# Performance work log

Measured on AMD Instinct MI355X. Metric: run time of the kernel, lower is better.

Reference implementation:

```python
import jax, jax.numpy as jnp
import numpy as np

EMB = 1024

def setup_inputs() -> dict:
    key = jax.random.key(0)
    ks = jax.random.split(key, 6)
    B, S, E = 4, 2048, EMB
    x = jax.random.normal(ks[0], (B, S, E), dtype=jnp.float32)
    attention_mask = jax.random.randint(ks[1], (B, S, S), 0, 2, dtype=jnp.int32)
    proj_w = jax.random.normal(ks[2], (E, 3 * E), dtype=jnp.float32) * (1.0 / np.sqrt(E))
    proj_b = jax.random.normal(ks[3], (3 * E,), dtype=jnp.float32) * 0.02
    out_w = jax.random.normal(ks[4], (E, E), dtype=jnp.float32) * (1.0 / np.sqrt(E))
    out_b = jax.random.normal(ks[5], (E,), dtype=jnp.float32) * 0.02
    return {"x": x, "attention_mask": attention_mask, "proj_w": proj_w,
            "proj_b": proj_b, "out_w": out_w, "out_b": out_b}

def reference(x, attention_mask, proj_w, proj_b, out_w, out_b):
    E = x.shape[-1]
    scale = 1.0 / jnp.sqrt(jnp.asarray(E, x.dtype))
    qkv = x @ proj_w + proj_b                      # [B,S,3E]
    q, k, v = jnp.split(qkv, 3, axis=-1)           # each [B,S,E]
    scores = jnp.einsum('bqe,bke->bqk', q, k) * scale  # [B,S,S]
    scores = jnp.where(attention_mask == 0, jnp.asarray(-1e20, scores.dtype), scores)
    attn = jax.nn.softmax(scores, axis=-1)
    ctx = jnp.einsum('bqk,bke->bqe', attn, v)      # [B,S,E]
    return ctx @ out_w + out_b
```

## Files before the change

### kernel.cpp

```cpp
#include <hip/hip_runtime.h>
#include <cstdint>

typedef unsigned short u16;
typedef uint32_t u32;
typedef __bf16 bf16x8 __attribute__((ext_vector_type(8)));
typedef float f32x4 __attribute__((ext_vector_type(4)));

__device__ __forceinline__ u16 f2bf(float f) {
  unsigned u = __float_as_uint(f);
  u += 0x7fffu + ((u >> 16) & 1u);
  return (u16)(u >> 16);
}

__device__ __forceinline__ void async16(const void* g, void* l) {
  __builtin_amdgcn_global_load_lds(
      (const __attribute__((address_space(1))) uint32_t*)g,
      (__attribute__((address_space(3))) uint32_t*)l, 16, 0, 0);
}

__global__ __launch_bounds__(256) void k_prep(const float* __restrict__ x, u16* __restrict__ xb,
                                              const float* __restrict__ pw, u16* __restrict__ wt,
                                              const float* __restrict__ ow, u16* __restrict__ owt,
                                              const int* __restrict__ mask, u32* __restrict__ mbits) {
  const int bid = blockIdx.x;
  if (bid < 8192) {
    const int i = bid * 256 + threadIdx.x;
    const float4 v = ((const float4*)x)[i];
    ushort4 o;
    o.x = f2bf(v.x); o.y = f2bf(v.y); o.z = f2bf(v.z); o.w = f2bf(v.w);
    ((ushort4*)xb)[i] = o;
    return;
  }
  if (bid >= 12288) {
    const size_t w = (size_t)(bid - 12288) * 256 + threadIdx.x;
    const int* p = mask + w * 32;
    u32 bits = 0;
#pragma unroll
    for (int j = 0; j < 8; ++j) {
      const int4 v = ((const int4*)p)[j];
      bits |= (u32)(v.x & 1) << (j * 4 + 0);
      bits |= (u32)(v.y & 1) << (j * 4 + 1);
      bits |= (u32)(v.z & 1) << (j * 4 + 2);
      bits |= (u32)(v.w & 1) << (j * 4 + 3);
    }
    mbits[w] = bits;
    return;
  }
  __shared__ u16 tile[32][33];
  const int tx = threadIdx.x & 31, ty = threadIdx.x >> 5;
  const float* in;
  u16* outp;
  int lda, ldo, c0, r0;
  if (bid < 11264) {
    const int id = bid - 8192;
    c0 = (id % 96) * 32; r0 = (id / 96) * 32;
    in = pw; outp = wt; lda = 3072; ldo = 1024;
  } else {
    const int id = bid - 11264;
    c0 = (id % 32) * 32; r0 = (id / 32) * 32;
    in = ow; outp = owt; lda = 1024; ldo = 1024;
  }
#pragma unroll
  for (int i = 0; i < 4; ++i)
    tile[ty + i * 8][tx] = f2bf(in[(size_t)(r0 + ty + i * 8) * lda + c0 + tx]);
  __syncthreads();
#pragma unroll
  for (int i = 0; i < 4; ++i)
    outp[(size_t)(c0 + ty + i * 8) * ldo + r0 + tx] = tile[tx][ty + i * 8];
}

template <int MODE>
__global__ __launch_bounds__(512, 2) void gemm256(
    const u16* __restrict__ A, long lda, long bsA,
    const u16* __restrict__ Bt, long ldb, long bsB,
    void* __restrict__ C, long ldc, long bsC,
    int M, int N, int K,
    const float* __restrict__ bias, const u32* __restrict__ mbits) {
  __shared__ u16 sm[4][2][8192];
  const int gx = gridDim.x, gxy = gridDim.x * gridDim.y;
  const int T = gxy * gridDim.z;
  int L = blockIdx.x + gx * blockIdx.y + gxy * blockIdx.z;
  L = (L & 7) * (T >> 3) + (L >> 3);
  const int b = L / gxy, rr = L % gxy, bx = rr % gx, by = rr / gx;
  const int m0 = by * 256, n0 = bx * 256;
  const int tid = threadIdx.x;
  const int lane = tid & 63;
  const int w = tid >> 6;
  const int wr = w >> 2, wc = w & 3;

  const int sl = tid >> 3;
  const int sgo = (tid & 7) ^ (sl & 7);
  const int srow = 2 * sl + (sgo >> 2);
  const int skoff = (sgo & 3) * 8;
  const u16* pa = A + (size_t)b * bsA + (size_t)(m0 + srow) * lda + skoff;
  const u16* pb = Bt + (size_t)b * bsB + (size_t)(n0 + srow) * ldb + skoff;
  const size_t a128 = (size_t)128 * lda, b128 = (size_t)128 * ldb;

  const int m_l = lane & 15, q = lane >> 4;
  const int l7 = m_l >> 1;
  const int g = (((m_l & 1) * 4) + q) ^ l7;
  const int aoff = wr * 4096 + l7 * 64 + g * 8;
  const int boff = wc * 2048 + l7 * 64 + g * 8;

  f32x4 acc[8][4] = {};

#define STAGE(tt)                                   \
  {                                                 \
    const int bi_ = (tt)&3;                         \
    const size_t ko_ = (size_t)(tt)*32;             \
    u16* da_ = &sm[bi_][0][0] + tid * 8;            \
    u16* db_ = &sm[bi_][1][0] + tid * 8;            \
    async16(pa + ko_, da_);                         \
    async16(pa + ko_ + a128, da_ + 4096);           \
    async16(pb + ko_, db_);                         \
    async16(pb + ko_ + b128, db_ + 4096);           \
  }

  const int NTL = K >> 5;
  STAGE(0) STAGE(1) STAGE(2)
  asm volatile("s_waitcnt vmcnt(8)" ::: "memory");
  __builtin_amdgcn_s_barrier();

  for (int t = 0; t < NTL; ++t) {
    const u16* ab = &sm[t & 3][0][0] + aoff;
    const u16* bb = &sm[t & 3][1][0] + boff;
    bf16x8 af[8], bf[4];
#pragma unroll
    for (int mt = 0; mt < 8; ++mt) af[mt] = *(const bf16x8*)(ab + mt * 512);
#pragma unroll
    for (int nt = 0; nt < 4; ++nt) bf[nt] = *(const bf16x8*)(bb + nt * 512);
    if (t + 3 < NTL) STAGE(t + 3)
    __builtin_amdgcn_s_setprio(1);
#pragma unroll
    for (int mt = 0; mt < 8; ++mt)
#pragma unroll
      for (int nt = 0; nt < 4; ++nt)
        acc[mt][nt] = __builtin_amdgcn_mfma_f32_16x16x32_bf16(af[mt], bf[nt], acc[mt][nt], 0, 0, 0);
    __builtin_amdgcn_s_setprio(0);
    __builtin_amdgcn_sched_barrier(0);
    if (t + 3 < NTL)
      asm volatile("s_waitcnt vmcnt(8)" ::: "memory");
    else if (t + 3 == NTL)
      asm volatile("s_waitcnt vmcnt(4)" ::: "memory");
    else if (t + 2 == NTL)
      asm volatile("s_waitcnt vmcnt(0)" ::: "memory");
    if (t + 1 < NTL) __builtin_amdgcn_s_barrier();
  }
#undef STAGE

  if constexpr (MODE == 1) {
    __syncthreads();
    u32* smw = (u32*)&sm[0][0][0];
    const int rl = tid >> 1, wo = (tid & 1) * 4;
    const uint4 mv = *(const uint4*)(mbits + ((size_t)b * M + m0 + rl) * (N >> 5) + (n0 >> 5) + wo);
    smw[rl * 8 + wo] = mv.x;
    smw[rl * 8 + wo + 1] = mv.y;
    smw[rl * 8 + wo + 2] = mv.z;
    smw[rl * 8 + wo + 3] = mv.w;
    __syncthreads();
  }

#pragma unroll
  for (int mt = 0; mt < 8; ++mt) {
#pragma unroll
    for (int nt = 0; nt < 4; ++nt) {
      const int col = n0 + wc * 64 + nt * 16 + m_l;
      const int row0 = m0 + wr * 128 + mt * 16 + q * 4;
#pragma unroll
      for (int r = 0; r < 4; ++r) {
        const int row = row0 + r;
        float v = acc[mt][nt][r];
        if constexpr (MODE == 0) {
          v += bias[col];
          if (col < 1024) v *= 0.03125f;
          ((u16*)C)[(size_t)b * bsC + (size_t)row * ldc + col] = f2bf(v);
        } else {
          const int cl = wc * 64 + nt * 16 + m_l;
          const int rl2 = wr * 128 + mt * 16 + q * 4 + r;
          const u32 wb = ((const u32*)&sm[0][0][0])[rl2 * 8 + (cl >> 5)];
          v = ((wb >> (cl & 31)) & 1u) ? __expf(fminf(v, 30.f)) : 0.f;
          ((u16*)C)[(size_t)b * bsC + (size_t)row * ldc + col] = f2bf(v);
        }
      }
    }
  }
}

template <int MODE, int TM, int BN>
__device__ __forceinline__ void gemm_core(
    u16* As, u16* Bs,
    const u16* __restrict__ A, long lda, long bsA,
    const u16* __restrict__ Bt, long ldb, long bsB,
    void* __restrict__ C, long ldc, long bsC,
    int M, int N, int K,
    const float* __restrict__ bias, const u32* __restrict__ mbits,
    int b, int bx, int by) {
  constexpr int MT = TM / 32, NT = BN / 32;
  constexpr int ACALLS = TM / 8, TOT = (TM + BN) / 8, NC = TOT / 4;
  const int m0 = by * TM, n0 = bx * BN;
  const int lane = threadIdx.x & 63;
  const int w = threadIdx.x >> 6;
  const int wr = w >> 1, wc = w & 1;

  const int srow = lane >> 3;
  const int scol = ((lane & 7) ^ ((lane >> 3) & 7)) * 8;
  const u16* pa = A + (size_t)b * bsA + (size_t)(m0 + srow) * lda + scol;
  const u16* pb = Bt + (size_t)b * bsB + (size_t)(n0 + srow) * ldb + scol;

  const int m_l = lane & 15, q = lane >> 4, m7 = m_l & 7;
  const int offs[2] = {(q ^ m7) * 8, ((4 + q) ^ m7) * 8};

  f32x4 acc[MT][NT] = {};
  f32x4 accs[MT] = {};
  bf16x8 ones;
#pragma unroll
  for (int e = 0; e < 8; ++e) ones[e] = (__bf16)1.0f;

  for (int kt = 0; kt < K; kt += 64) {
    __syncthreads();
#pragma unroll
    for (int g = 0; g < NC; ++g) {
      const int idx = w * NC + g;
      if (idx < ACALLS)
        async16(pa + (size_t)(idx * 8) * lda, As + idx * 512);
      else
        async16(pb + (size_t)((idx - ACALLS) * 8) * ldb, Bs + (idx - ACALLS) * 512);
    }
    __syncthreads();
#pragma unroll
    for (int s = 0; s < 2; ++s) {
      bf16x8 af[MT], bfr[NT];
#pragma unroll
      for (int t = 0; t < MT; ++t)
        af[t] = *(const bf16x8*)(As + (wr * (TM / 2) + t * 16 + m_l) * 64 + offs[s]);
#pragma unroll
      for (int t = 0; t < NT; ++t)
        bfr[t] = *(const bf16x8*)(Bs + (wc * (BN / 2) + t * 16 + m_l) * 64 + offs[s]);
#pragma unroll
      for (int mt = 0; mt < MT; ++mt)
#pragma unroll
        for (int nt = 0; nt < NT; ++nt)
          acc[mt][nt] = __builtin_amdgcn_mfma_f32_16x16x32_bf16(af[mt], bfr[nt], acc[mt][nt], 0, 0, 0);
      if constexpr (MODE == 2) {
#pragma unroll
        for (int mt = 0; mt < MT; ++mt)
          accs[mt] = __builtin_amdgcn_mfma_f32_16x16x32_bf16(af[mt], ones, accs[mt], 0, 0, 0);
      }
    }
    pa += 64;
    pb += 64;
  }

  float rinv[MT][4];
  if constexpr (MODE == 2) {
#pragma unroll
    for (int mt = 0; mt < MT; ++mt)
#pragma unroll
      for (int r = 0; r < 4; ++r) rinv[mt][r] = 1.0f / accs[mt][r];
  }

#pragma unroll
  for (int mt = 0; mt < MT; ++mt) {
#pragma unroll
    for (int nt = 0; nt < NT; ++nt) {
      const int col = n0 + wc * (BN / 2) + nt * 16 + m_l;
      const int row0 = m0 + wr * (TM / 2) + mt * 16 + q * 4;
      if constexpr (MODE == 3) {
        ushort4 o;
        o.x = f2bf(acc[mt][nt][0]); o.y = f2bf(acc[mt][nt][1]);
        o.z = f2bf(acc[mt][nt][2]); o.w = f2bf(acc[mt][nt][3]);
        *(ushort4*)((u16*)C + (size_t)b * bsC + (size_t)col * ldc + row0) = o;
      } else {
#pragma unroll
        for (int r = 0; r < 4; ++r) {
          const int row = row0 + r;
          float v = acc[mt][nt][r];
          if constexpr (MODE == 2) {
            v = v * rinv[mt][r] + bias[col];
            ((float*)C)[(size_t)b * bsC + (size_t)row * ldc + col] = v;
          }
        }
      }
    }
  }
}

template <int MODE, int TM, int BN>
__global__ __launch_bounds__(256) void gemm_bt(
    const u16* __restrict__ A, long lda, long bsA,
    const u16* __restrict__ Bt, long ldb, long bsB,
    void* __restrict__ C, long ldc, long bsC,
    int M, int N, int K,
    const float* __restrict__ bias, const u32* __restrict__ mbits) {
  __shared__ u16 As[TM * 64];
  __shared__ u16 Bs[BN * 64];
  const int gx = gridDim.x, gxy = gridDim.x * gridDim.y;
  const int T = gxy * gridDim.z;
  int L = blockIdx.x + gx * blockIdx.y + gxy * blockIdx.z;
  L = (L & 7) * (T >> 3) + (L >> 3);
  const int bz = L / gxy, r = L % gxy;
  gemm_core<MODE, TM, BN>(As, Bs, A, lda, bsA, Bt, ldb, bsB, C, ldc, bsC, M, N, K,
                          bias, mbits, bz, r % gx, r / gx);
}

extern "C" void kernel_launch(void* const* d_in, const int* in_sizes, int n_in,
                              void* d_out, int out_size, void* d_ws, size_t ws_size,
                              hipStream_t stream) {
  const float* x = (const float*)d_in[0];
  const int* mask = (const int*)d_in[1];
  const float* proj_w = (const float*)d_in[2];
  const float* proj_b = (const float*)d_in[3];
  const float* out_w = (const float*)d_in[4];
  const float* out_b = (const float*)d_in[5];
  float* out = (float*)d_out;

  char* ws = (char*)d_ws;
  u16* xb = (u16*)(ws);
  u16* wt = (u16*)(ws + 16777216);
  u16* owt = (u16*)(ws + 23068672);
  u16* qkv = (u16*)(ws + 25165824);
  u16* P = (u16*)(ws + 75497472);
  u32* mbits = (u32*)(ws + 109051904);
  u16* Ut = (u16*)xb;

  k_prep<<<14336, 256, 0, stream>>>(x, xb, proj_w, wt, out_w, owt, mask, mbits);
  gemm256<0><<<dim3(12, 32, 1), 512, 0, stream>>>(
      xb, 1024, 0, wt, 1024, 0, qkv, 3072, 0, 8192, 3072, 1024, proj_b, nullptr);
  gemm256<1><<<dim3(8, 8, 4), 512, 0, stream>>>(
      qkv, 3072, (long)2048 * 3072, qkv + 1024, 3072, (long)2048 * 3072,
      P, 2048, (long)2048 * 2048, 2048, 2048, 1024, nullptr, mbits);
  gemm_bt<3, 64, 128><<<dim3(8, 32, 4), 256, 0, stream>>>(
      qkv + 2048, 3072, (long)2048 * 3072, owt, 1024, 0,
      Ut, 2048, (long)1024 * 2048, 2048, 1024, 1024, nullptr, nullptr);
  gemm_bt<2, 128, 128><<<dim3(8, 16, 4), 256, 0, stream>>>(
      P, 2048, (long)2048 * 2048, Ut, 2048, (long)1024 * 2048,
      out, 1024, (long)2048 * 1024, 2048, 1024, 2048, out_b, nullptr);
}
```

Before: 322.3 us.

## Split GEMM main loop into four phases interleaving LDS reads, async loads and MFMAs

Restructures the K-loop of the bf16 GEMM into four phases. Each phase reads two A fragments from LDS, issues one quarter of the next stage's global-to-LDS loads, and runs eight MFMAs, with a barrier before and after each phase. The aim is to spread memory traffic across the MFMA stream and cut register pressure from holding all eight A fragments at once. In exchange it adds many more workgroup barriers per iteration, which can stall waves.

```diff
diff --git a/kernel.cpp b/kernel.cpp
--- a/kernel.cpp
+++ b/kernel.cpp
@@ -104,49 +104,64 @@
 
   f32x4 acc[8][4] = {};
 
-#define STAGE(tt)                                   \
-  {                                                 \
-    const int bi_ = (tt)&3;                         \
-    const size_t ko_ = (size_t)(tt)*32;             \
-    u16* da_ = &sm[bi_][0][0] + tid * 8;            \
-    u16* db_ = &sm[bi_][1][0] + tid * 8;            \
-    async16(pa + ko_, da_);                         \
-    async16(pa + ko_ + a128, da_ + 4096);           \
-    async16(pb + ko_, db_);                         \
-    async16(pb + ko_ + b128, db_ + 4096);           \
+#define MFMA_(A_, B_, C_) __builtin_amdgcn_mfma_f32_16x16x32_bf16(A_, B_, C_, 0, 0, 0)
+#define STAGE1(tt) { async16(pa + (size_t)(tt)*32, &sm[(tt)&3][0][0] + tid * 8); }
+#define STAGE2(tt) { async16(pa + (size_t)(tt)*32 + a128, &sm[(tt)&3][0][0] + tid * 8 + 4096); }
+#define STAGE3(tt) { async16(pb + (size_t)(tt)*32, &sm[(tt)&3][1][0] + tid * 8); }
+#define STAGE4(tt) { async16(pb + (size_t)(tt)*32 + b128, &sm[(tt)&3][1][0] + tid * 8 + 4096); }
+
+#define PHASE(p, STG, TAIL)                                        \
+  {                                                                \
+    bf16x8 afa = *(const bf16x8*)(ab + (2 * (p)) * 512);           \
+    bf16x8 afb = *(const bf16x8*)(ab + (2 * (p) + 1) * 512);       \
+    STG;                                                           \
+    __builtin_amdgcn_s_barrier();                                  \
+    asm volatile("s_waitcnt lgkmcnt(0)" ::: "memory");             \
+    __builtin_amdgcn_sched_barrier(0);                             \
+    __builtin_amdgcn_s_setprio(1);                                 \
+    acc[2 * (p)][0] = MFMA_(afa, bf0, acc[2 * (p)][0]);            \
+    acc[2 * (p)][1] = MFMA_(afa, bf1, acc[2 * (p)][1]);            \
+    acc[2 * (p)][2] = MFMA_(afa, bf2, acc[2 * (p)][2]);            \
+    acc[2 * (p)][3] = MFMA_(afa, bf3, acc[2 * (p)][3]);            \
+    acc[2 * (p) + 1][0] = MFMA_(afb, bf0, acc[2 * (p) + 1][0]);    \
+    acc[2 * (p) + 1][1] = MFMA_(afb, bf1, acc[2 * (p) + 1][1]);    \
+    acc[2 * (p) + 1][2] = MFMA_(afb, bf2, acc[2 * (p) + 1][2]);    \
+    acc[2 * (p) + 1][3] = MFMA_(afb, bf3, acc[2 * (p) + 1][3]);    \
+    __builtin_amdgcn_s_setprio(0);                                 \
+    __builtin_amdgcn_sched_barrier(0);                             \
+    TAIL;                                                          \
+    __builtin_amdgcn_s_barrier();                                  \
   }
 
   const int NTL = K >> 5;
-  STAGE(0) STAGE(1) STAGE(2)
+  STAGE1(0) STAGE2(0) STAGE3(0) STAGE4(0)
+  STAGE1(1) STAGE2(1) STAGE3(1) STAGE4(1)
+  STAGE1(2) STAGE2(2) STAGE3(2) STAGE4(2)
   asm volatile("s_waitcnt vmcnt(8)" ::: "memory");
   __builtin_amdgcn_s_barrier();
 
   for (int t = 0; t < NTL; ++t) {
     const u16* ab = &sm[t & 3][0][0] + aoff;
     const u16* bb = &sm[t & 3][1][0] + boff;
-    bf16x8 af[8], bf[4];
-#pragma unroll
-    for (int mt = 0; mt < 8; ++mt) af[mt] = *(const bf16x8*)(ab + mt * 512);
-#pragma unroll
-    for (int nt = 0; nt < 4; ++nt) bf[nt] = *(const bf16x8*)(bb + nt * 512);
-    if (t + 3 < NTL) STAGE(t + 3)
-    __builtin_amdgcn_s_setprio(1);
-#pragma unroll
-    for (int mt = 0; mt < 8; ++mt)
-#pragma unroll
-      for (int nt = 0; nt < 4; ++nt)
-        acc[mt][nt] = __builtin_amdgcn_mfma_f32_16x16x32_bf16(af[mt], bf[nt], acc[mt][nt], 0, 0, 0);
-    __builtin_amdgcn_s_setprio(0);
-    __builtin_amdgcn_sched_barrier(0);
-    if (t + 3 < NTL)
-      asm volatile("s_waitcnt vmcnt(8)" ::: "memory");
-    else if (t + 3 == NTL)
-      asm volatile("s_waitcnt vmcnt(4)" ::: "memory");
-    else if (t + 2 == NTL)
-      asm volatile("s_waitcnt vmcnt(0)" ::: "memory");
-    if (t + 1 < NTL) __builtin_amdgcn_s_barrier();
-  }
-#undef STAGE
+    const bool st = (t + 3 < NTL);
+    bf16x8 bf0 = *(const bf16x8*)(bb);
+    bf16x8 bf1 = *(const bf16x8*)(bb + 512);
+    bf16x8 bf2 = *(const bf16x8*)(bb + 1024);
+    bf16x8 bf3 = *(const bf16x8*)(bb + 1536);
+    PHASE(0, if (st) STAGE1(t + 3), )
+    PHASE(1, if (st) STAGE2(t + 3), )
+    PHASE(2, if (st) STAGE3(t + 3), )
+    PHASE(3, if (st) STAGE4(t + 3),
+          if (st) { asm volatile("s_waitcnt vmcnt(8)" ::: "memory"); }
+          else if (t + 3 == NTL) { asm volatile("s_waitcnt vmcnt(4)" ::: "memory"); }
+          else if (t + 2 == NTL) { asm volatile("s_waitcnt vmcnt(0)" ::: "memory"); })
+  }
+#undef PHASE
+#undef STAGE1
+#undef STAGE2
+#undef STAGE3
+#undef STAGE4
+#undef MFMA_
 
   if constexpr (MODE == 1) {
     __syncthreads();
```

New measurement: 338.6 us. +5.1%, slower.

## Double-buffer LDS fragment reads in registers to overlap with MFMA

Applied to the files above, without the earlier changes.

Restructures the GEMM main loop into a two-way unrolled ping-pong. Each iteration issues the LDS reads for the next K-tile into a second register set before running the MFMAs on the current tile, so shared-memory read latency hides behind matrix math. The cost is doubled fragment registers, which may lower occupancy. It also adds a redundant LDS read on the final iteration and assumes an even tile count.

```diff
diff --git a/kernel.cpp b/kernel.cpp
--- a/kernel.cpp
+++ b/kernel.cpp
@@ -103,7 +103,9 @@
   const int boff = wc * 2048 + l7 * 64 + g * 8;
 
   f32x4 acc[8][4] = {};
-
+  bf16x8 a0[8], b0[4], a1[8], b1[4];
+
+#define MFMA_(A_, B_, C_) __builtin_amdgcn_mfma_f32_16x16x32_bf16(A_, B_, C_, 0, 0, 0)
 #define STAGE(tt)                                   \
   {                                                 \
     const int bi_ = (tt)&3;                         \
@@ -115,38 +117,52 @@
     async16(pb + ko_, db_);                         \
     async16(pb + ko_ + b128, db_ + 4096);           \
   }
+#define READ(NA, NB, tt)                                          \
+  {                                                               \
+    const u16* ab_ = &sm[(tt)&3][0][0] + aoff;                    \
+    const u16* bb_ = &sm[(tt)&3][1][0] + boff;                    \
+    _Pragma("unroll") for (int mt = 0; mt < 8; ++mt)              \
+        NA[mt] = *(const bf16x8*)(ab_ + mt * 512);                \
+    _Pragma("unroll") for (int nt = 0; nt < 4; ++nt)              \
+        NB[nt] = *(const bf16x8*)(bb_ + nt * 512);                \
+  }
+#define ITER(t, CA, CB, NA, NB)                              \
+  {                                                          \
+    asm volatile("s_waitcnt lgkmcnt(0)" ::: "memory");       \
+    __builtin_amdgcn_sched_barrier(0);                       \
+    if ((t) + 3 < NTL) STAGE((t) + 3)                        \
+    if ((t) + 3 < NTL) {                                     \
+      asm volatile("s_waitcnt vmcnt(8)" ::: "memory");       \
+    } else if ((t) + 3 == NTL) {                             \
+      asm volatile("s_waitcnt vmcnt(4)" ::: "memory");       \
+    } else if ((t) + 2 == NTL) {                             \
+      asm volatile("s_waitcnt vmcnt(0)" ::: "memory");       \
+    }                                                        \
+    if ((t) + 1 < NTL) __builtin_amdgcn_s_barrier();         \
+    READ(NA, NB, (t) + 1)                                    \
+    __builtin_amdgcn_sched_barrier(0);                       \
+    __builtin_amdgcn_s_setprio(1);                           \
+    _Pragma("unroll") for (int mt = 0; mt < 8; ++mt)         \
+        _Pragma("unroll") for (int nt = 0; nt < 4; ++nt)     \
+            acc[mt][nt] = MFMA_(CA[mt], CB[nt], acc[mt][nt]);\
+    __builtin_amdgcn_s_setprio(0);                           \
+    __builtin_amdgcn_sched_barrier(0);                       \
+  }
 
   const int NTL = K >> 5;
   STAGE(0) STAGE(1) STAGE(2)
   asm volatile("s_waitcnt vmcnt(8)" ::: "memory");
   __builtin_amdgcn_s_barrier();
-
-  for (int t = 0; t < NTL; ++t) {
-    const u16* ab = &sm[t & 3][0][0] + aoff;
-    const u16* bb = &sm[t & 3][1][0] + boff;
-    bf16x8 af[8], bf[4];
-#pragma unroll
-    for (int mt = 0; mt < 8; ++mt) af[mt] = *(const bf16x8*)(ab + mt * 512);
-#pragma unroll
-    for (int nt = 0; nt < 4; ++nt) bf[nt] = *(const bf16x8*)(bb + nt * 512);
-    if (t + 3 < NTL) STAGE(t + 3)
-    __builtin_amdgcn_s_setprio(1);
-#pragma unroll
-    for (int mt = 0; mt < 8; ++mt)
-#pragma unroll
-      for (int nt = 0; nt < 4; ++nt)
-        acc[mt][nt] = __builtin_amdgcn_mfma_f32_16x16x32_bf16(af[mt], bf[nt], acc[mt][nt], 0, 0, 0);
-    __builtin_amdgcn_s_setprio(0);
-    __builtin_amdgcn_sched_barrier(0);
-    if (t + 3 < NTL)
-      asm volatile("s_waitcnt vmcnt(8)" ::: "memory");
-    else if (t + 3 == NTL)
-      asm volatile("s_waitcnt vmcnt(4)" ::: "memory");
-    else if (t + 2 == NTL)
-      asm volatile("s_waitcnt vmcnt(0)" ::: "memory");
-    if (t + 1 < NTL) __builtin_amdgcn_s_barrier();
-  }
+  READ(a0, b0, 0)
+
+  for (int t = 0; t < NTL; t += 2) {
+    ITER(t, a0, b0, a1, b1)
+    ITER(t + 1, a1, b1, a0, b0)
+  }
+#undef ITER
+#undef READ
 #undef STAGE
+#undef MFMA_
 
   if constexpr (MODE == 1) {
     __syncthreads();
```

Measured after the change: 318.2 us. No clear change (-1.3%).

## Shrink gemm256 tile to 256x128 with 3-stage pipeline for higher occupancy

Applied to the files above, without the earlier changes.

Changes the 256x256 gemm256 tile to 256x128 with an 8-warp 4x2 layout, cutting per-thread accumulators in half. The LDS buffering goes from 4 stages to 3, with rotating buffer indices and adjusted vmcnt waits, and launch bounds ask for 4 blocks per CU. Grids double to match the narrower tiles. The goal is more resident waves and more blocks per GEMM to hide latency and fill the CUs, at the cost of less operand reuse per tile and a shallower prefetch.

```diff
diff --git a/kernel.cpp b/kernel.cpp
--- a/kernel.cpp
+++ b/kernel.cpp
@@ -70,23 +70,23 @@
 }
 
 template <int MODE>
-__global__ __launch_bounds__(512, 2) void gemm256(
+__global__ __launch_bounds__(512, 4) void gemm256(
     const u16* __restrict__ A, long lda, long bsA,
     const u16* __restrict__ Bt, long ldb, long bsB,
     void* __restrict__ C, long ldc, long bsC,
     int M, int N, int K,
     const float* __restrict__ bias, const u32* __restrict__ mbits) {
-  __shared__ u16 sm[4][2][8192];
+  __shared__ u16 sm[3][12288];
   const int gx = gridDim.x, gxy = gridDim.x * gridDim.y;
   const int T = gxy * gridDim.z;
   int L = blockIdx.x + gx * blockIdx.y + gxy * blockIdx.z;
   L = (L & 7) * (T >> 3) + (L >> 3);
   const int b = L / gxy, rr = L % gxy, bx = rr % gx, by = rr / gx;
-  const int m0 = by * 256, n0 = bx * 256;
+  const int m0 = by * 256, n0 = bx * 128;
   const int tid = threadIdx.x;
   const int lane = tid & 63;
   const int w = tid >> 6;
-  const int wr = w >> 2, wc = w & 3;
+  const int wr = w >> 1, wc = w & 1;
 
   const int sl = tid >> 3;
   const int sgo = (tid & 7) ^ (sl & 7);
@@ -94,78 +94,79 @@
   const int skoff = (sgo & 3) * 8;
   const u16* pa = A + (size_t)b * bsA + (size_t)(m0 + srow) * lda + skoff;
   const u16* pb = Bt + (size_t)b * bsB + (size_t)(n0 + srow) * ldb + skoff;
-  const size_t a128 = (size_t)128 * lda, b128 = (size_t)128 * ldb;
+  const size_t a128 = (size_t)128 * lda;
 
   const int m_l = lane & 15, q = lane >> 4;
   const int l7 = m_l >> 1;
   const int g = (((m_l & 1) * 4) + q) ^ l7;
-  const int aoff = wr * 4096 + l7 * 64 + g * 8;
-  const int boff = wc * 2048 + l7 * 64 + g * 8;
-
-  f32x4 acc[8][4] = {};
-
-#define STAGE(tt)                                   \
+  const int aoff = wr * 2048 + l7 * 64 + g * 8;
+  const int boff = 8192 + wc * 2048 + l7 * 64 + g * 8;
+
+  f32x4 acc[4][4] = {};
+
+#define MFMA_(A_, B_, C_) __builtin_amdgcn_mfma_f32_16x16x32_bf16(A_, B_, C_, 0, 0, 0)
+#define STAGE(tt, bi)                               \
   {                                                 \
-    const int bi_ = (tt)&3;                         \
     const size_t ko_ = (size_t)(tt)*32;             \
-    u16* da_ = &sm[bi_][0][0] + tid * 8;            \
-    u16* db_ = &sm[bi_][1][0] + tid * 8;            \
+    u16* da_ = &sm[bi][0] + tid * 8;                \
     async16(pa + ko_, da_);                         \
     async16(pa + ko_ + a128, da_ + 4096);           \
-    async16(pb + ko_, db_);                         \
-    async16(pb + ko_ + b128, db_ + 4096);           \
+    async16(pb + ko_, &sm[bi][8192] + tid * 8);     \
   }
 
   const int NTL = K >> 5;
-  STAGE(0) STAGE(1) STAGE(2)
-  asm volatile("s_waitcnt vmcnt(8)" ::: "memory");
+  STAGE(0, 0) STAGE(1, 1)
+  asm volatile("s_waitcnt vmcnt(3)" ::: "memory");
   __builtin_amdgcn_s_barrier();
 
+  int br = 0, bs = 2;
   for (int t = 0; t < NTL; ++t) {
-    const u16* ab = &sm[t & 3][0][0] + aoff;
-    const u16* bb = &sm[t & 3][1][0] + boff;
-    bf16x8 af[8], bf[4];
-#pragma unroll
-    for (int mt = 0; mt < 8; ++mt) af[mt] = *(const bf16x8*)(ab + mt * 512);
+    if (t + 2 < NTL) STAGE(t + 2, bs)
+    const u16* ab = &sm[br][0] + aoff;
+    const u16* bb = &sm[br][0] + boff;
+    bf16x8 af[4], bf[4];
+#pragma unroll
+    for (int mt = 0; mt < 4; ++mt) af[mt] = *(const bf16x8*)(ab + mt * 512);
 #pragma unroll
     for (int nt = 0; nt < 4; ++nt) bf[nt] = *(const bf16x8*)(bb + nt * 512);
-    if (t + 3 < NTL) STAGE(t + 3)
+    asm volatile("s_waitcnt lgkmcnt(0)" ::: "memory");
+    __builtin_amdgcn_sched_barrier(0);
     __builtin_amdgcn_s_setprio(1);
 #pragma unroll
-    for (int mt = 0; mt < 8; ++mt)
+    for (int mt = 0; mt < 4; ++mt)
 #pragma unroll
       for (int nt = 0; nt < 4; ++nt)
-        acc[mt][nt] = __builtin_amdgcn_mfma_f32_16x16x32_bf16(af[mt], bf[nt], acc[mt][nt], 0, 0, 0);
+        acc[mt][nt] = MFMA_(af[mt], bf[nt], acc[mt][nt]);
     __builtin_amdgcn_s_setprio(0);
     __builtin_amdgcn_sched_barrier(0);
-    if (t + 3 < NTL)
-      asm volatile("s_waitcnt vmcnt(8)" ::: "memory");
-    else if (t + 3 == NTL)
-      asm volatile("s_waitcnt vmcnt(4)" ::: "memory");
-    else if (t + 2 == NTL)
+    if (t + 2 < NTL) {
+      asm volatile("s_waitcnt vmcnt(3)" ::: "memory");
+    } else if (t + 1 < NTL) {
       asm volatile("s_waitcnt vmcnt(0)" ::: "memory");
+    }
     if (t + 1 < NTL) __builtin_amdgcn_s_barrier();
+    br = (br == 2) ? 0 : br + 1;
+    bs = (bs == 2) ? 0 : bs + 1;
   }
 #undef STAGE
+#undef MFMA_
 
   if constexpr (MODE == 1) {
     __syncthreads();
-    u32* smw = (u32*)&sm[0][0][0];
-    const int rl = tid >> 1, wo = (tid & 1) * 4;
-    const uint4 mv = *(const uint4*)(mbits + ((size_t)b * M + m0 + rl) * (N >> 5) + (n0 >> 5) + wo);
-    smw[rl * 8 + wo] = mv.x;
-    smw[rl * 8 + wo + 1] = mv.y;
-    smw[rl * 8 + wo + 2] = mv.z;
-    smw[rl * 8 + wo + 3] = mv.w;
+    u32* smw = (u32*)&sm[0][0];
+    const int rl = tid >> 1, pr = tid & 1;
+    const uint2 mv = *(const uint2*)(mbits + ((size_t)b * M + m0 + rl) * (N >> 5) + (n0 >> 5) + pr * 2);
+    smw[rl * 4 + pr * 2] = mv.x;
+    smw[rl * 4 + pr * 2 + 1] = mv.y;
     __syncthreads();
   }
 
 #pragma unroll
-  for (int mt = 0; mt < 8; ++mt) {
+  for (int mt = 0; mt < 4; ++mt) {
 #pragma unroll
     for (int nt = 0; nt < 4; ++nt) {
       const int col = n0 + wc * 64 + nt * 16 + m_l;
-      const int row0 = m0 + wr * 128 + mt * 16 + q * 4;
+      const int row0 = m0 + wr * 64 + mt * 16 + q * 4;
 #pragma unroll
       for (int r = 0; r < 4; ++r) {
         const int row = row0 + r;
@@ -176,8 +177,8 @@
           ((u16*)C)[(size_t)b * bsC + (size_t)row * ldc + col] = f2bf(v);
         } else {
           const int cl = wc * 64 + nt * 16 + m_l;
-          const int rl2 = wr * 128 + mt * 16 + q * 4 + r;
-          const u32 wb = ((const u32*)&sm[0][0][0])[rl2 * 8 + (cl >> 5)];
+          const int rl2 = wr * 64 + mt * 16 + q * 4 + r;
+          const u32 wb = ((const u32*)&sm[0][0])[rl2 * 4 + (cl >> 5)];
           v = ((wb >> (cl & 31)) & 1u) ? __expf(fminf(v, 30.f)) : 0.f;
           ((u16*)C)[(size_t)b * bsC + (size_t)row * ldc + col] = f2bf(v);
         }
@@ -324,9 +325,9 @@
   u16* Ut = (u16*)xb;
 
   k_prep<<<14336, 256, 0, stream>>>(x, xb, proj_w, wt, out_w, owt, mask, mbits);
-  gemm256<0><<<dim3(12, 32, 1), 512, 0, stream>>>(
+  gemm256<0><<<dim3(24, 32, 1), 512, 0, stream>>>(
       xb, 1024, 0, wt, 1024, 0, qkv, 3072, 0, 8192, 3072, 1024, proj_b, nullptr);
-  gemm256<1><<<dim3(8, 8, 4), 512, 0, stream>>>(
+  gemm256<1><<<dim3(16, 8, 4), 512, 0, stream>>>(
       qkv, 3072, (long)2048 * 3072, qkv + 1024, 3072, (long)2048 * 3072,
       P, 2048, (long)2048 * 2048, 2048, 2048, 1024, nullptr, mbits);
   gemm_bt<3, 64, 128><<<dim3(8, 32, 4), 256, 0, stream>>>(
```

Result: no change. 317.9 us (-1.4%).
